# Kernel optimization log

Hardware: AMD Instinct MI355X
Metric: run time of the kernel (lower is better)

## Reference

```python
import jax, jax.numpy as jnp
import numpy as np

B, C, H, W = 2, 256, 200, 200   # feature map (stride-4 BEV head)
N = 512                          # number of rotated RoIs
PH, PW = 7, 7                    # pooled output bins
SCALE = 0.25                     # spatial_scale
RATIO = 2                        # sampling_ratio (grid per bin)


def setup_inputs() -> dict:
    key = jax.random.key(0)
    k1, k2, k3, k4, k5 = jax.random.split(key, 5)
    inputs = jax.random.normal(k1, (B, C, H, W), dtype=jnp.float32)
    # rois: (batch_idx, cx, cy, w, h, theta) in image coords (feature coords / SCALE)
    bidx = jax.random.randint(k2, (N,), 0, B).astype(jnp.float32)
    centers = jax.random.uniform(k3, (N, 2), jnp.float32, 60.0, H / SCALE - 60.0)
    wh = jax.random.uniform(k4, (N, 2), jnp.float32, 20.0, 120.0)
    ang = jax.random.uniform(k5, (N, 1), jnp.float32, -np.pi, np.pi)
    rois = jnp.concatenate([bidx[:, None], centers, wh, ang], axis=1)
    return {"inputs": inputs, "rois": rois}


def _rotated_roi_align(inputs, rois):
    Bc, Cc, Hc, Wc = inputs.shape
    b = rois[:, 0].astype(jnp.int32)                       # [N]
    cx = rois[:, 1] * SCALE
    cy = rois[:, 2] * SCALE
    rw = jnp.maximum(rois[:, 3] * SCALE, 1.0)
    rh = jnp.maximum(rois[:, 4] * SCALE, 1.0)
    theta = rois[:, 5]
    cos_t = jnp.cos(theta)[:, None, None, None, None]
    sin_t = jnp.sin(theta)[:, None, None, None, None]

    bin_h = (rh / PH)[:, None, None, None, None]           # [N,1,1,1,1]
    bin_w = (rw / PW)[:, None, None, None, None]
    ph = jnp.arange(PH, dtype=jnp.float32)[None, :, None, None, None]
    pw = jnp.arange(PW, dtype=jnp.float32)[None, None, :, None, None]
    gy = ((jnp.arange(RATIO, dtype=jnp.float32) + 0.5) / RATIO)[None, None, None, :, None]
    gx = ((jnp.arange(RATIO, dtype=jnp.float32) + 0.5) / RATIO)[None, None, None, None, :]

    # local (un-rotated) sample coords relative to roi center -> [N,PH,PW,G,G]
    yy = -rh[:, None, None, None, None] / 2 + (ph + gy) * bin_h
    xx = -rw[:, None, None, None, None] / 2 + (pw + gx) * bin_w
    # rotate and translate into feature-map coords
    y = yy * cos_t - xx * sin_t + cy[:, None, None, None, None]
    x = yy * sin_t + xx * cos_t + cx[:, None, None, None, None]
    y = jnp.broadcast_to(y, (rois.shape[0], PH, PW, RATIO, RATIO))
    x = jnp.broadcast_to(x, (rois.shape[0], PH, PW, RATIO, RATIO))

    valid = (y > -1.0) & (y < Hc) & (x > -1.0) & (x < Wc)
    y = jnp.maximum(y, 0.0)
    x = jnp.maximum(x, 0.0)

    yl = jnp.floor(y).astype(jnp.int32)
    xl = jnp.floor(x).astype(jnp.int32)
    hi_y = yl >= Hc - 1
    hi_x = xl >= Wc - 1
    yl = jnp.minimum(yl, Hc - 1)
    xl = jnp.minimum(xl, Wc - 1)
    yh = jnp.where(hi_y, Hc - 1, yl + 1)
    xh = jnp.where(hi_x, Wc - 1, xl + 1)
    y = jnp.where(hi_y, yl.astype(y.dtype), y)
    x = jnp.where(hi_x, xl.astype(x.dtype), x)

    ly = y - yl.astype(y.dtype)
    lx = x - xl.astype(x.dtype)
    hy = 1.0 - ly
    hx = 1.0 - lx

    flat = inputs.reshape(Bc, Cc, Hc * Wc)
    bb = b[:, None, None, None, None]

    def gather(yy_i, xx_i):
        # -> [N,PH,PW,G,G,C]
        return flat[bb, :, yy_i * Wc + xx_i]

    val = ((hy * hx)[..., None] * gather(yl, xl)
           + (hy * lx)[..., None] * gather(yl, xh)
           + (ly * hx)[..., None] * gather(yh, xl)
           + (ly * lx)[..., None] * gather(yh, xh))
    val = jnp.where(valid[..., None], val, 0.0)
    out = val.mean(axis=(3, 4))                            # [N,PH,PW,C]
    return jnp.transpose(out, (0, 3, 1, 2))                # [N,C,PH,PW]


def reference(inputs, rois):
    return _rotated_roi_align(inputs, rois)
```

## Files before the change

kernel.cpp:

```cpp
#include <hip/hip_runtime.h>

#define Bc   2
#define Cc   256
#define Hc   200
#define Wc   200
#define NROI 512
#define NBIN 49
#define HWn  (Hc * Wc)
#define LSTRIDE 260

__device__ inline unsigned short f2bf(float f) {
    unsigned int u = __float_as_uint(f);
    return (unsigned short)((u + 0x7FFFu + ((u >> 16) & 1u)) >> 16);
}
__device__ inline float bf2f(unsigned short u) {
    return __uint_as_float(((unsigned int)u) << 16);
}

struct RoiParams { int b; float cx, cy, rw, rh, cs, sn, bh, bw; };

__device__ inline RoiParams load_roi(const float* rois, int n) {
    RoiParams p;
    const float* r = rois + n * 6;
    p.b  = (int)r[0];
    p.cx = r[1] * 0.25f;  p.cy = r[2] * 0.25f;
    p.rw = fmaxf(r[3] * 0.25f, 1.0f);
    p.rh = fmaxf(r[4] * 0.25f, 1.0f);
    p.cs = cosf(r[5]);    p.sn = sinf(r[5]);
    p.bh = p.rh * (1.0f / 7.0f);
    p.bw = p.rw * (1.0f / 7.0f);
    return p;
}

__device__ inline void sample_wix(const RoiParams& p, int ph, int pw, int s,
                                  float* wt, int* pix) {
    const float sy = (s >> 1) ? 0.75f : 0.25f;
    const float sx = (s & 1)  ? 0.75f : 0.25f;
    const float yy = -0.5f * p.rh + ((float)ph + sy) * p.bh;
    const float xx = -0.5f * p.rw + ((float)pw + sx) * p.bw;
    float y = yy * p.cs - xx * p.sn + p.cy;
    float x = yy * p.sn + xx * p.cs + p.cx;
    const bool valid = (y > -1.0f) && (y < (float)Hc) && (x > -1.0f) && (x < (float)Wc);
    y = fmaxf(y, 0.0f); x = fmaxf(x, 0.0f);
    int yl = (int)y, xl = (int)x;
    const bool hiy = yl >= Hc - 1, hix = xl >= Wc - 1;
    yl = min(yl, Hc - 1); xl = min(xl, Wc - 1);
    const int yh = hiy ? (Hc - 1) : (yl + 1);
    const int xh = hix ? (Wc - 1) : (xl + 1);
    const float ly = hiy ? 0.0f : (y - (float)yl);
    const float lx = hix ? 0.0f : (x - (float)xl);
    const float hy = 1.0f - ly, hx = 1.0f - lx;
    const float vm = valid ? 0.25f : 0.0f;
    wt[0] = vm * hy * hx;  wt[1] = vm * hy * lx;
    wt[2] = vm * ly * hx;  wt[3] = vm * ly * lx;
    const int rl = (p.b * Hc + yl) * Wc;
    const int rt = (p.b * Hc + yh) * Wc;
    pix[0] = rl + xl;  pix[1] = rl + xh;
    pix[2] = rt + xl;  pix[3] = rt + xh;
}

__global__ __launch_bounds__(256) void transpose_to_bf16_nhwc(const float* __restrict__ in,
                                                              unsigned short* __restrict__ out) {
    __shared__ unsigned short tile[64][65];
    const int b   = blockIdx.z;
    const int hw0 = blockIdx.x * 64;
    const int c0  = blockIdx.y * 64;
    const int tx  = threadIdx.x & 63;
    const int ty  = threadIdx.x >> 6;

    #pragma unroll
    for (int i = ty; i < 64; i += 4) {
        float v = in[(size_t)(b * Cc + c0 + i) * HWn + hw0 + tx];
        tile[i][tx] = f2bf(v);
    }
    __syncthreads();

    const int j  = threadIdx.x & 31;
    const int r0 = threadIdx.x >> 5;
    unsigned int* out32 = (unsigned int*)out;
    #pragma unroll
    for (int r = r0; r < 64; r += 8) {
        unsigned int lo = tile[2 * j][r];
        unsigned int hi = tile[2 * j + 1][r];
        out32[((size_t)(b * HWn + hw0 + r) * Cc + c0) / 2 + j] = lo | (hi << 16);
    }
}

template <int NB, int B0>
__device__ void consume_part(const ushort4* __restrict__ f4, const RoiParams& p,
                             float* sbuf, int t) {
    const int w  = t >> 6;
    const int cq = t & 63;
    for (int bl = w; bl < NB; bl += 4) {
        const int bin = B0 + bl;
        const int ph = bin / 7;
        const int pw = bin - ph * 7;

        float wt[16];
        int   ix[16];
        #pragma unroll
        for (int s = 0; s < 4; ++s) {
            float wts[4]; int pix[4];
            sample_wix(p, ph, pw, s, wts, pix);
            #pragma unroll
            for (int k = 0; k < 4; ++k) {
                wt[s * 4 + k] = wts[k];
                ix[s * 4 + k] = pix[k] * 64 + cq;
            }
        }

        ushort4 v[16];
        #pragma unroll
        for (int i = 0; i < 16; ++i) v[i] = f4[ix[i]];

        float ax = 0.f, ay = 0.f, az = 0.f, aw = 0.f;
        #pragma unroll
        for (int i = 0; i < 16; ++i) {
            ax += wt[i] * bf2f(v[i].x);
            ay += wt[i] * bf2f(v[i].y);
            az += wt[i] * bf2f(v[i].z);
            aw += wt[i] * bf2f(v[i].w);
        }

        float4 res; res.x = ax; res.y = ay; res.z = az; res.w = aw;
        *(float4*)(&sbuf[bl * LSTRIDE + cq * 4]) = res;
    }
}

template <int NB, int B0>
__device__ void writeout_part(float* __restrict__ out, const float* sbuf, int n, int t) {
    const size_t obase = (size_t)n * (Cc * NBIN);
    for (int e = t; e < Cc * NB; e += 256) {
        const int c  = e / NB;
        const int bi = e - c * NB;
        out[obase + (size_t)c * NBIN + B0 + bi] = sbuf[bi * LSTRIDE + c];
    }
}

__global__ __launch_bounds__(256, 4) void roialign_bf16(const unsigned short* __restrict__ feat,
                                                        const float* __restrict__ rois,
                                                        float* __restrict__ out) {
    __shared__ float sbuf[13 * LSTRIDE];

    const int bid = blockIdx.x;
    const int q   = bid >> 3;
    const int n   = ((q >> 2) << 3) | (bid & 7);
    const int j   = q & 3;
    const int t   = threadIdx.x;

    const RoiParams p = load_roi(rois, n);
    const ushort4* f4 = (const ushort4*)feat;

    if (j == 0)      consume_part<12,  0>(f4, p, sbuf, t);
    else if (j == 1) consume_part<12, 12>(f4, p, sbuf, t);
    else if (j == 2) consume_part<12, 24>(f4, p, sbuf, t);
    else             consume_part<13, 36>(f4, p, sbuf, t);

    __syncthreads();

    if (j == 0)      writeout_part<12,  0>(out, sbuf, n, t);
    else if (j == 1) writeout_part<12, 12>(out, sbuf, n, t);
    else if (j == 2) writeout_part<12, 24>(out, sbuf, n, t);
    else             writeout_part<13, 36>(out, sbuf, n, t);
}

__global__ __launch_bounds__(256) void roialign_nchw(const float* __restrict__ feat,
                                                     const float* __restrict__ rois,
                                                     float* __restrict__ out) {
    __shared__ float sbuf[NBIN * LSTRIDE];
    const int n = blockIdx.x, t = threadIdx.x;
    const int g = t >> 6, cq = t & 63;
    const RoiParams p = load_roi(rois, n);
    for (int bin = g; bin < NBIN; bin += 4) {
        const int ph = bin / 7, pw = bin - ph * 7;
        float acc[4] = {0.f, 0.f, 0.f, 0.f};
        for (int s = 0; s < 4; ++s) {
            float wts[4]; int pix[4];
            sample_wix(p, ph, pw, s, wts, pix);
            #pragma unroll
            for (int i = 0; i < 4; ++i) {
                const size_t cb = (size_t)(p.b * Cc + cq * 4 + i) * HWn;
                acc[i] += wts[0] * feat[cb + pix[0] - p.b * HWn] +
                          wts[1] * feat[cb + pix[1] - p.b * HWn] +
                          wts[2] * feat[cb + pix[2] - p.b * HWn] +
                          wts[3] * feat[cb + pix[3] - p.b * HWn];
            }
        }
        #pragma unroll
        for (int i = 0; i < 4; ++i) sbuf[bin * LSTRIDE + cq * 4 + i] = acc[i];
    }
    __syncthreads();
    const size_t obase = (size_t)n * (Cc * NBIN);
    for (int e = t; e < Cc * NBIN; e += 256) {
        const int c = e / NBIN, bi = e - c * NBIN;
        out[obase + e] = sbuf[bi * LSTRIDE + c];
    }
}

extern "C" void kernel_launch(void* const* d_in, const int* in_sizes, int n_in,
                              void* d_out, int out_size, void* d_ws, size_t ws_size,
                              hipStream_t stream) {
    const float* inputs = (const float*)d_in[0];
    const float* rois   = (const float*)d_in[1];
    float* out = (float*)d_out;

    const size_t need = (size_t)Bc * HWn * Cc * sizeof(unsigned short);
    if (d_ws != nullptr && ws_size >= need) {
        unsigned short* nhwc = (unsigned short*)d_ws;
        dim3 tg(HWn / 64, Cc / 64, Bc);
        transpose_to_bf16_nhwc<<<tg, 256, 0, stream>>>(inputs, nhwc);
        roialign_bf16<<<NROI * 4, 256, 0, stream>>>(nhwc, rois, out);
    } else {
        roialign_nchw<<<NROI, 256, 0, stream>>>(inputs, rois, out);
    }
}
```

Measured before the change: 48.11 us.

## Sort RoIs by batch and y-band and process one RoI per 512-thread block

Adds a small kernel that bucket-sorts RoIs by batch index and vertical band, then maps blocks through this permutation so concurrently running blocks touch nearby feature rows and share L2 lines. The RoI-align kernel drops the four-way bin split and instead gives each RoI one 512-thread block that covers all 49 bins, writing the output contiguously. This costs an extra kernel launch, a larger LDS footprint per block and fewer blocks in total. The work per RoI is no longer spread across blocks, so occupancy and balance may suffer.

```diff
diff --git a/kernel.cpp b/kernel.cpp
--- a/kernel.cpp
+++ b/kernel.cpp
@@ -8,6 +8,7 @@
 #define NBIN 49
 #define HWn  (Hc * Wc)
 #define LSTRIDE 260
+#define MAP_BYTES ((size_t)Bc * HWn * Cc * 2)
 
 __device__ inline unsigned short f2bf(float f) {
     unsigned int u = __float_as_uint(f);
@@ -59,6 +60,33 @@
     pix[2] = rt + xl;  pix[3] = rt + xh;
 }
 
+__global__ __launch_bounds__(512) void sort_rois(const float* __restrict__ rois,
+                                                 int* __restrict__ perm) {
+    __shared__ int hist[256];
+    __shared__ int base[256];
+    const int t = threadIdx.x;
+    if (t < 256) hist[t] = 0;
+    __syncthreads();
+
+    const float* r = rois + t * 6;
+    const int   b  = (int)r[0];
+    const float cy = r[2] * 0.25f;
+    int band = (int)(cy * (127.0f / 200.0f));
+    band = min(max(band, 0), 127);
+    const int bucket = b * 128 + band;
+    atomicAdd(&hist[bucket], 1);
+    __syncthreads();
+
+    if (t == 0) {
+        int acc = 0;
+        for (int i = 0; i < 256; ++i) { base[i] = acc; acc += hist[i]; }
+    }
+    __syncthreads();
+
+    const int rank = atomicAdd(&base[bucket], 1);
+    perm[rank] = t;
+}
+
 __global__ __launch_bounds__(256) void transpose_to_bf16_nhwc(const float* __restrict__ in,
                                                               unsigned short* __restrict__ out) {
     __shared__ unsigned short tile[64][65];
@@ -86,13 +114,22 @@
     }
 }
 
-template <int NB, int B0>
-__device__ void consume_part(const ushort4* __restrict__ f4, const RoiParams& p,
-                             float* sbuf, int t) {
-    const int w  = t >> 6;
-    const int cq = t & 63;
-    for (int bl = w; bl < NB; bl += 4) {
-        const int bin = B0 + bl;
+__global__ __launch_bounds__(512, 4) void roialign_bf16(const unsigned short* __restrict__ feat,
+                                                        const float* __restrict__ rois,
+                                                        const int* __restrict__ perm,
+                                                        float* __restrict__ out) {
+    __shared__ float sbuf[NBIN * LSTRIDE];
+
+    const int bid = blockIdx.x;
+    const int n   = perm[((bid & 7) << 6) | (bid >> 3)];
+    const int t   = threadIdx.x;
+    const int w   = t >> 6;
+    const int cq  = t & 63;
+
+    const RoiParams p = load_roi(rois, n);
+    const ushort4* f4 = (const ushort4*)feat;
+
+    for (int bin = w; bin < NBIN; bin += 8) {
         const int ph = bin / 7;
         const int pw = bin - ph * 7;
 
@@ -123,45 +160,17 @@
         }
 
         float4 res; res.x = ax; res.y = ay; res.z = az; res.w = aw;
-        *(float4*)(&sbuf[bl * LSTRIDE + cq * 4]) = res;
-    }
-}
-
-template <int NB, int B0>
-__device__ void writeout_part(float* __restrict__ out, const float* sbuf, int n, int t) {
+        *(float4*)(&sbuf[bin * LSTRIDE + cq * 4]) = res;
+    }
+
+    __syncthreads();
+
     const size_t obase = (size_t)n * (Cc * NBIN);
-    for (int e = t; e < Cc * NB; e += 256) {
-        const int c  = e / NB;
-        const int bi = e - c * NB;
-        out[obase + (size_t)c * NBIN + B0 + bi] = sbuf[bi * LSTRIDE + c];
-    }
-}
-
-__global__ __launch_bounds__(256, 4) void roialign_bf16(const unsigned short* __restrict__ feat,
-                                                        const float* __restrict__ rois,
-                                                        float* __restrict__ out) {
-    __shared__ float sbuf[13 * LSTRIDE];
-
-    const int bid = blockIdx.x;
-    const int q   = bid >> 3;
-    const int n   = ((q >> 2) << 3) | (bid & 7);
-    const int j   = q & 3;
-    const int t   = threadIdx.x;
-
-    const RoiParams p = load_roi(rois, n);
-    const ushort4* f4 = (const ushort4*)feat;
-
-    if (j == 0)      consume_part<12,  0>(f4, p, sbuf, t);
-    else if (j == 1) consume_part<12, 12>(f4, p, sbuf, t);
-    else if (j == 2) consume_part<12, 24>(f4, p, sbuf, t);
-    else             consume_part<13, 36>(f4, p, sbuf, t);
-
-    __syncthreads();
-
-    if (j == 0)      writeout_part<12,  0>(out, sbuf, n, t);
-    else if (j == 1) writeout_part<12, 12>(out, sbuf, n, t);
-    else if (j == 2) writeout_part<12, 24>(out, sbuf, n, t);
-    else             writeout_part<13, 36>(out, sbuf, n, t);
+    for (int e = t; e < Cc * NBIN; e += 512) {
+        const int c  = e / NBIN;
+        const int bi = e - c * NBIN;
+        out[obase + e] = sbuf[bi * LSTRIDE + c];
+    }
 }
 
 __global__ __launch_bounds__(256) void roialign_nchw(const float* __restrict__ feat,
@@ -204,12 +213,14 @@
     const float* rois   = (const float*)d_in[1];
     float* out = (float*)d_out;
 
-    const size_t need = (size_t)Bc * HWn * Cc * sizeof(unsigned short);
+    const size_t need = MAP_BYTES + NROI * sizeof(int);
     if (d_ws != nullptr && ws_size >= need) {
         unsigned short* nhwc = (unsigned short*)d_ws;
+        int* perm = (int*)((char*)d_ws + MAP_BYTES);
+        sort_rois<<<1, 512, 0, stream>>>(rois, perm);
         dim3 tg(HWn / 64, Cc / 64, Bc);
         transpose_to_bf16_nhwc<<<tg, 256, 0, stream>>>(inputs, nhwc);
-        roialign_bf16<<<NROI * 4, 256, 0, stream>>>(nhwc, rois, out);
+        roialign_bf16<<<NROI, 512, 0, stream>>>(nhwc, rois, perm, out);
     } else {
         roialign_nchw<<<NROI, 256, 0, stream>>>(inputs, rois, out);
     }
```

Result: slower. 50.47 us (+4.9%).

## Process one RoI per 512-thread block and use nontemporal output stores

Applied to the files above, without the earlier changes.

The bf16 RoI-align kernel now gives each RoI to a single 512-thread block holding all 49 bins in shared memory, replacing four 256-thread blocks per RoI that each handled a slice of the bins. Each block can then write its output contiguously in one pass instead of four strided partial writes. Output stores use nontemporal hints so the large output does not pollute the cache. The trade-off is fewer blocks (512, about two per CU on a 256-CU device) and much more shared memory per block, which may limit occupancy and latency hiding.

```diff
diff --git a/kernel.cpp b/kernel.cpp
--- a/kernel.cpp
+++ b/kernel.cpp
@@ -86,13 +86,20 @@
     }
 }
 
-template <int NB, int B0>
-__device__ void consume_part(const ushort4* __restrict__ f4, const RoiParams& p,
-                             float* sbuf, int t) {
+__global__ __launch_bounds__(512, 4) void roialign_bf16(const unsigned short* __restrict__ feat,
+                                                        const float* __restrict__ rois,
+                                                        float* __restrict__ out) {
+    __shared__ float sbuf[NBIN * LSTRIDE];
+
+    const int n  = blockIdx.x;
+    const int t  = threadIdx.x;
     const int w  = t >> 6;
     const int cq = t & 63;
-    for (int bl = w; bl < NB; bl += 4) {
-        const int bin = B0 + bl;
+
+    const RoiParams p = load_roi(rois, n);
+    const ushort4* f4 = (const ushort4*)feat;
+
+    for (int bin = w; bin < NBIN; bin += 8) {
         const int ph = bin / 7;
         const int pw = bin - ph * 7;
 
@@ -123,45 +130,17 @@
         }
 
         float4 res; res.x = ax; res.y = ay; res.z = az; res.w = aw;
-        *(float4*)(&sbuf[bl * LSTRIDE + cq * 4]) = res;
+        *(float4*)(&sbuf[bin * LSTRIDE + cq * 4]) = res;
     }
-}
-
-template <int NB, int B0>
-__device__ void writeout_part(float* __restrict__ out, const float* sbuf, int n, int t) {
-    const size_t obase = (size_t)n * (Cc * NBIN);
-    for (int e = t; e < Cc * NB; e += 256) {
-        const int c  = e / NB;
-        const int bi = e - c * NB;
-        out[obase + (size_t)c * NBIN + B0 + bi] = sbuf[bi * LSTRIDE + c];
-    }
-}
-
-__global__ __launch_bounds__(256, 4) void roialign_bf16(const unsigned short* __restrict__ feat,
-                                                        const float* __restrict__ rois,
-                                                        float* __restrict__ out) {
-    __shared__ float sbuf[13 * LSTRIDE];
-
-    const int bid = blockIdx.x;
-    const int q   = bid >> 3;
-    const int n   = ((q >> 2) << 3) | (bid & 7);
-    const int j   = q & 3;
-    const int t   = threadIdx.x;
-
-    const RoiParams p = load_roi(rois, n);
-    const ushort4* f4 = (const ushort4*)feat;
-
-    if (j == 0)      consume_part<12,  0>(f4, p, sbuf, t);
-    else if (j == 1) consume_part<12, 12>(f4, p, sbuf, t);
-    else if (j == 2) consume_part<12, 24>(f4, p, sbuf, t);
-    else             consume_part<13, 36>(f4, p, sbuf, t);
 
     __syncthreads();
 
-    if (j == 0)      writeout_part<12,  0>(out, sbuf, n, t);
-    else if (j == 1) writeout_part<12, 12>(out, sbuf, n, t);
-    else if (j == 2) writeout_part<12, 24>(out, sbuf, n, t);
-    else             writeout_part<13, 36>(out, sbuf, n, t);
+    const size_t obase = (size_t)n * (Cc * NBIN);
+    for (int e = t; e < Cc * NBIN; e += 512) {
+        const int c  = e / NBIN;
+        const int bi = e - c * NBIN;
+        __builtin_nontemporal_store(sbuf[bi * LSTRIDE + c], &out[obase + e]);
+    }
 }
 
 __global__ __launch_bounds__(256) void roialign_nchw(const float* __restrict__ feat,
@@ -193,7 +172,7 @@
     const size_t obase = (size_t)n * (Cc * NBIN);
     for (int e = t; e < Cc * NBIN; e += 256) {
         const int c = e / NBIN, bi = e - c * NBIN;
-        out[obase + e] = sbuf[bi * LSTRIDE + c];
+        __builtin_nontemporal_store(sbuf[bi * LSTRIDE + c], &out[obase + e]);
     }
 }
 
@@ -209,7 +188,7 @@
         unsigned short* nhwc = (unsigned short*)d_ws;
         dim3 tg(HWn / 64, Cc / 64, Bc);
         transpose_to_bf16_nhwc<<<tg, 256, 0, stream>>>(inputs, nhwc);
-        roialign_bf16<<<NROI * 4, 256, 0, stream>>>(nhwc, rois, out);
+        roialign_bf16<<<NROI, 512, 0, stream>>>(nhwc, rois, out);
     } else {
         roialign_nchw<<<NROI, 256, 0, stream>>>(inputs, rois, out);
     }
```

After: 45.56 us. -5.3%, faster.
